# Optimization experiments

Hardware: AMD Instinct MI355X
Metric: run time of the kernel (lower is better)

The kernel has to match this reference:

```python
import jax, jax.numpy as jnp
import numpy as np
from jax import lax

B, T, V, D, H, C = 256, 1024, 5000, 100, 64, 2


def setup_inputs() -> dict:
    key = jax.random.key(0)
    k0, k1, k2, k3, k4 = jax.random.split(key, 5)
    tokens = jax.random.randint(k0, (B, T), 0, V)  # 0 is the mask/pad id
    E = jax.random.normal(k1, (V, D), dtype=jnp.float32) * 0.05
    W = jax.random.normal(k2, (D, H), dtype=jnp.float32) * (1.0 / np.sqrt(D))
    U = jax.random.normal(k3, (H, H), dtype=jnp.float32) * (1.0 / np.sqrt(H))
    b = jnp.zeros((H,), dtype=jnp.float32)
    Wd = jax.random.normal(k4, (H, C), dtype=jnp.float32) * (1.0 / np.sqrt(H))
    bd = jnp.zeros((C,), dtype=jnp.float32)
    return {"tokens": tokens, "E": E, "W": W, "U": U, "b": b, "Wd": Wd, "bd": bd}


def reference(tokens, E, W, U, b, Wd, bd):
    # Embedding with mask_zero=True: mask where token != 0
    x = E[tokens]                      # [B, T, D]
    mask = tokens != 0                 # [B, T] bool
    # Precompute input projection for all timesteps (batched GEMM).
    xW = jnp.einsum('btd,dh->bth', x, W) + b  # [B, T, H]

    def step(h, inp):
        xw_t, m_t = inp                # xw_t: [B,H], m_t: [B]
        h_new = jnp.tanh(xw_t + h @ U)
        # Keras masked recurrence: masked steps carry previous state/output.
        h = jnp.where(m_t[:, None], h_new, h)
        return h, h

    h0 = jnp.zeros((tokens.shape[0], U.shape[0]), dtype=xW.dtype)
    _, hs = lax.scan(step, h0, (jnp.swapaxes(xW, 0, 1), mask.T))  # hs: [T, B, H]
    hs = jnp.swapaxes(hs, 0, 1)        # [B, T, H]
    pooled = jnp.mean(hs, axis=1)      # tf.reduce_mean over time (unmasked mean)
    # Dropout is identity at inference.
    logits = pooled @ Wd + bd
    return jax.nn.sigmoid(logits)
```

## Files before the change

### kernel.cpp

```cpp
#include <hip/hip_runtime.h>

#define B_ 256
#define T_ 1024
#define V_ 5000
#define D_ 100
#define H_ 64
#define C_ 2

__global__ __launch_bounds__(256) void ew_kernel(const float* __restrict__ E,
                                                 const float* __restrict__ W,
                                                 const float* __restrict__ bias,
                                                 float* __restrict__ EW) {
    int idx = blockIdx.x * 256 + threadIdx.x;
    if (idx >= V_ * H_) return;
    int h = idx & (H_ - 1);
    int v = idx >> 6;
    float acc = bias[h];
    const float* Erow = E + v * D_;
    #pragma unroll 4
    for (int d = 0; d < D_; ++d) {
        acc = fmaf(Erow[d], W[d * H_ + h], acc);
    }
    EW[idx] = acc;
}

__device__ __forceinline__ float readlane_f(float v, int lane) {
    return __uint_as_float(__builtin_amdgcn_readlane(__float_as_uint(v), lane));
}

__global__ __launch_bounds__(64, 1) void rnn_kernel(const int* __restrict__ tokens,
                                                    const float* __restrict__ EW,
                                                    const float* __restrict__ U,
                                                    const float* __restrict__ Wd,
                                                    const float* __restrict__ bd,
                                                    float* __restrict__ out) {
    const int b = blockIdx.x;
    const int j = threadIdx.x;

    __shared__ int sh_tok[T_ + 2];

    float u[H_];
    #pragma unroll
    for (int k = 0; k < H_; ++k) {
        u[k] = U[k * H_ + j];
    }

    const int* tok = tokens + b * T_;
    #pragma unroll
    for (int k = 0; k < T_ / H_; ++k) {
        sh_tok[k * H_ + j] = tok[k * H_ + j];
    }
    if (j < 2) sh_tok[T_ + j] = 0;
    __syncthreads();

    float h = 0.f;
    float pooled = 0.f;

    int2 tkA = *(const int2*)&sh_tok[0];
    float xw0 = EW[tkA.x * H_ + j];
    float xw1 = EW[tkA.y * H_ + j];

    #define RNN_STEP(tokv, xwv)                                          \
    {                                                                    \
        float a0 = 0.f, a1 = 0.f, a2 = 0.f, a3 = 0.f;                    \
        _Pragma("unroll")                                                \
        for (int c = 0; c < 16; ++c) {                                   \
            a0 = fmaf(readlane_f(h, 4 * c + 0), u[4 * c + 0], a0);       \
            a1 = fmaf(readlane_f(h, 4 * c + 1), u[4 * c + 1], a1);       \
            a2 = fmaf(readlane_f(h, 4 * c + 2), u[4 * c + 2], a2);       \
            a3 = fmaf(readlane_f(h, 4 * c + 3), u[4 * c + 3], a3);       \
        }                                                                \
        float x = ((a0 + a1) + (a2 + a3)) + (xwv);                       \
        float e = __expf(2.f * x);                                       \
        float r = __builtin_amdgcn_rcpf(e + 1.f);                        \
        float hn = fmaf(-2.f, r, 1.f);                                   \
        h = ((tokv) != 0) ? hn : h;                                      \
        pooled += h;                                                     \
    }

    for (int t = 0; t < T_; t += 2) {
        int2 tkB = *(const int2*)&sh_tok[t + 2];
        float xw2 = EW[tkB.x * H_ + j];
        float xw3 = EW[tkB.y * H_ + j];

        RNN_STEP(tkA.x, xw0);
        RNN_STEP(tkA.y, xw1);

        tkA = tkB;
        xw0 = xw2;
        xw1 = xw3;
    }
    #undef RNN_STEP

    float p = pooled * (1.0f / (float)T_);
    float v0 = p * Wd[j * C_ + 0];
    float v1 = p * Wd[j * C_ + 1];
    #pragma unroll
    for (int off = 32; off >= 1; off >>= 1) {
        v0 += __shfl_down(v0, off, 64);
        v1 += __shfl_down(v1, off, 64);
    }
    if (j == 0) {
        float l0 = v0 + bd[0];
        float l1 = v1 + bd[1];
        out[b * C_ + 0] = 1.f / (1.f + __expf(-l0));
        out[b * C_ + 1] = 1.f / (1.f + __expf(-l1));
    }
}

extern "C" void kernel_launch(void* const* d_in, const int* in_sizes, int n_in,
                              void* d_out, int out_size, void* d_ws, size_t ws_size,
                              hipStream_t stream) {
    const int*   tokens = (const int*)  d_in[0];
    const float* E      = (const float*)d_in[1];
    const float* W      = (const float*)d_in[2];
    const float* U      = (const float*)d_in[3];
    const float* bias   = (const float*)d_in[4];
    const float* Wd     = (const float*)d_in[5];
    const float* bd     = (const float*)d_in[6];
    float* out = (float*)d_out;
    float* EW  = (float*)d_ws;

    ew_kernel<<<(V_ * H_ + 255) / 256, 256, 0, stream>>>(E, W, bias, EW);
    rnn_kernel<<<B_, H_, 0, stream>>>(tokens, EW, U, Wd, bd, out);
}
```

Before: 348.4 us.

## Replace readlane broadcast matvec with DPP row-rotate systolic matvec and prescaled exp2 tanh

The recurrent h@U product now uses DPP wave rotates and one ds_bpermute to circulate h across lanes. U is loaded in matching rotated order as two half-streams, replacing 64 scalar readlanes per step, which serialize through SGPRs. U and the precomputed input projection are prescaled by 2/ln2 so tanh can use exp2 directly, and xw folds into the accumulator init. It relies on a runtime-detected DPP rotate direction (0x13C) and asm barriers to keep U in registers, so a wrong assumption about the rotation semantics would give incorrect results.

After: 383.4 us. +10.1%, slower.

```diff
diff --git a/kernel.cpp b/kernel.cpp
--- a/kernel.cpp
+++ b/kernel.cpp
@@ -6,6 +6,10 @@
 #define D_ 100
 #define H_ 64
 #define C_ 2
+
+typedef float f32x4 __attribute__((ext_vector_type(4)));
+
+#define SCALE_ 2.885390081777927f
 
 __global__ __launch_bounds__(256) void ew_kernel(const float* __restrict__ E,
                                                  const float* __restrict__ W,
@@ -21,12 +25,11 @@
     for (int d = 0; d < D_; ++d) {
         acc = fmaf(Erow[d], W[d * H_ + h], acc);
     }
-    EW[idx] = acc;
+    EW[idx] = SCALE_ * acc;
 }
 
-__device__ __forceinline__ float readlane_f(float v, int lane) {
-    return __uint_as_float(__builtin_amdgcn_readlane(__float_as_uint(v), lane));
-}
+#define ROT1(x) __int_as_float(__builtin_amdgcn_mov_dpp(                      \
+                    __float_as_int(x), 0x13C , 0xF, 0xF, false))
 
 __global__ __launch_bounds__(64, 1) void rnn_kernel(const int* __restrict__ tokens,
                                                     const float* __restrict__ EW,
@@ -39,11 +42,21 @@
 
     __shared__ int sh_tok[T_ + 2];
 
-    float u[H_];
+    int dir = __builtin_amdgcn_readfirstlane(
+                  __builtin_amdgcn_mov_dpp(j, 0x13C, 0xF, 0xF, false));
+
+    f32x4 uqA[8], uqB[8];
     #pragma unroll
-    for (int k = 0; k < H_; ++k) {
-        u[k] = U[k * H_ + j];
+    for (int m = 0; m < 32; ++m) {
+        int rowA = (j + dir * m) & 63;
+        int rowB = (rowA + 32) & 63;
+        uqA[m >> 2][m & 3] = SCALE_ * U[rowA * H_ + j];
+        uqB[m >> 2][m & 3] = SCALE_ * U[rowB * H_ + j];
     }
+    asm volatile("" : "+v"(uqA[0]), "+v"(uqA[1]), "+v"(uqA[2]), "+v"(uqA[3]),
+                      "+v"(uqA[4]), "+v"(uqA[5]), "+v"(uqA[6]), "+v"(uqA[7]),
+                      "+v"(uqB[0]), "+v"(uqB[1]), "+v"(uqB[2]), "+v"(uqB[3]),
+                      "+v"(uqB[4]), "+v"(uqB[5]), "+v"(uqB[6]), "+v"(uqB[7]));
 
     const int* tok = tokens + b * T_;
     #pragma unroll
@@ -52,6 +65,8 @@
     }
     if (j < 2) sh_tok[T_ + j] = 0;
     __syncthreads();
+
+    const int x32a = (j ^ 32) << 2;
 
     float h = 0.f;
     float pooled = 0.f;
@@ -62,23 +77,33 @@
 
     #define RNN_STEP(tokv, xwv)                                          \
     {                                                                    \
-        float a0 = 0.f, a1 = 0.f, a2 = 0.f, a3 = 0.f;                    \
+        float r1 = h;                                                    \
+        float r2 = __int_as_float(__builtin_amdgcn_ds_bpermute(          \
+                       x32a, __float_as_int(h)));                        \
+        float a0 = (xwv), a1 = 0.f;                                      \
         _Pragma("unroll")                                                \
-        for (int c = 0; c < 16; ++c) {                                   \
-            a0 = fmaf(readlane_f(h, 4 * c + 0), u[4 * c + 0], a0);       \
-            a1 = fmaf(readlane_f(h, 4 * c + 1), u[4 * c + 1], a1);       \
-            a2 = fmaf(readlane_f(h, 4 * c + 2), u[4 * c + 2], a2);       \
-            a3 = fmaf(readlane_f(h, 4 * c + 3), u[4 * c + 3], a3);       \
+        for (int l = 0; l < 31; ++l) {                                   \
+            a0 = fmaf(r1, uqA[l >> 2][l & 3], a0);                       \
+            r1 = ROT1(r1);                                               \
+            a1 = fmaf(r2, uqB[l >> 2][l & 3], a1);                       \
+            r2 = ROT1(r2);                                               \
         }                                                                \
-        float x = ((a0 + a1) + (a2 + a3)) + (xwv);                       \
-        float e = __expf(2.f * x);                                       \
-        float r = __builtin_amdgcn_rcpf(e + 1.f);                        \
+        a0 = fmaf(r1, uqA[7][3], a0);                                    \
+        a1 = fmaf(r2, uqB[7][3], a1);                                    \
+        float x2 = a0 + a1;                                              \
+        float ef = __builtin_amdgcn_exp2f(x2);                           \
+        float r = __builtin_amdgcn_rcpf(ef + 1.f);                       \
         float hn = fmaf(-2.f, r, 1.f);                                   \
         h = ((tokv) != 0) ? hn : h;                                      \
         pooled += h;                                                     \
     }
 
     for (int t = 0; t < T_; t += 2) {
+        asm volatile("" :: "v"(uqA[0]), "v"(uqA[1]), "v"(uqA[2]), "v"(uqA[3]),
+                           "v"(uqA[4]), "v"(uqA[5]), "v"(uqA[6]), "v"(uqA[7]),
+                           "v"(uqB[0]), "v"(uqB[1]), "v"(uqB[2]), "v"(uqB[3]),
+                           "v"(uqB[4]), "v"(uqB[5]), "v"(uqB[6]), "v"(uqB[7]));
+
         int2 tkB = *(const int2*)&sh_tok[t + 2];
         float xw2 = EW[tkB.x * H_ + j];
         float xw3 = EW[tkB.y * H_ + j];
```
